# Optimization experiments

Hardware: AMD Instinct MI355X
Metric: run time of the kernel (lower is better)

Reference implementation:

```python
import jax, jax.numpy as jnp
import numpy as np

DIM = 768
N_HEADS = 12
HEAD_DIM = DIM // N_HEADS
SCALE = HEAD_DIM ** -0.5


def setup_inputs() -> dict:
    key = jax.random.key(0)
    ks = jax.random.split(key, 5)
    B, N = 8, 1024
    x = jax.random.normal(ks[0], (B, N, DIM), dtype=jnp.float32)
    # Linear weights stored as (in, out) for x @ W; torch stores (out, in).
    w_qkv = jax.random.normal(ks[1], (DIM, 3 * DIM), dtype=jnp.float32) * (DIM ** -0.5)
    b_qkv = jnp.zeros((3 * DIM,), dtype=jnp.float32)
    w_proj = jax.random.normal(ks[2], (DIM, DIM), dtype=jnp.float32) * (DIM ** -0.5)
    b_proj = jnp.zeros((DIM,), dtype=jnp.float32)
    return {"x": x, "w_qkv": w_qkv, "b_qkv": b_qkv, "w_proj": w_proj, "b_proj": b_proj}


def reference(x, w_qkv, b_qkv, w_proj, b_proj):
    B, N, _ = x.shape
    qkv = x @ w_qkv + b_qkv                       # [B, N, 3*dim]
    qkv = qkv.reshape(B, N, 3, N_HEADS, HEAD_DIM)
    qkv = jnp.transpose(qkv, (2, 0, 3, 1, 4))     # [3, B, H, N, hd]
    q, k, v = qkv[0], qkv[1], qkv[2]
    attn = jnp.einsum("bhqd,bhkd->bhqk", q, k) * SCALE
    attn = jax.nn.softmax(attn, axis=-1)
    out = jnp.einsum("bhqk,bhkd->bhqd", attn, v)  # [B, H, N, hd]
    out = jnp.transpose(out, (0, 2, 1, 3)).reshape(B, N, DIM)
    return out @ w_proj + b_proj
```

## Files before the change

kernel.cpp:

```cpp
#include <hip/hip_runtime.h>
#include <cstdint>

#define DIM 768
#define NH 12
#define HD 64
#define SEQ 1024
#define NBH 96

#define QOFF  ((size_t)0)
#define KOFF  ((size_t)6291456)
#define VOFF  ((size_t)12582912)
#define AOFF  ((size_t)18874368)
#define XOFF  ((size_t)25165824)
#define WQOFF ((size_t)31457280)
#define WPOFF ((size_t)33226752)

#define QSCALE 0.18033688f

#define WAIT_VM8   __builtin_amdgcn_s_waitcnt(0x0F78)
#define WAIT_VM0   __builtin_amdgcn_s_waitcnt(0x0F70)
#define WAIT_LGKM0 __builtin_amdgcn_s_waitcnt(0xC07F)
#define BAR        __builtin_amdgcn_s_barrier()
#define CFENCE     __asm__ __volatile__("" ::: "memory")

typedef __attribute__((ext_vector_type(8))) __bf16 bf16x8;
typedef __attribute__((ext_vector_type(4))) float f32x4;
typedef unsigned short u16;

__device__ __forceinline__ u16 f2bf(float f) {
    union { float f; unsigned u; } x; x.f = f;
    unsigned r = x.u + 0x7fffu + ((x.u >> 16) & 1u);
    return (u16)(r >> 16);
}

__device__ __forceinline__ void async_cp16(const void* g, void* l) {
    __builtin_amdgcn_global_load_lds((const __attribute__((address_space(1))) void*)g,
                                     (__attribute__((address_space(3))) void*)l, 16, 0, 0);
}

__global__ __launch_bounds__(256) void prep(const float* __restrict__ x,
                                            const float* __restrict__ wq,
                                            const float* __restrict__ wp,
                                            u16* __restrict__ ws) {
    const int bid = blockIdx.x;
    const int tid = threadIdx.x;
    if (bid < 6144) {
        int i = bid * 256 + tid;
        float4 v = *(const float4*)&x[(size_t)i * 4];
        ushort4 o; o.x = f2bf(v.x); o.y = f2bf(v.y); o.z = f2bf(v.z); o.w = f2bf(v.w);
        *(ushort4*)&ws[XOFF + (size_t)i * 4] = o;
        return;
    }
    __shared__ float T[64][65];
    const float* w; u16* wt; int N, bx, by;
    if (bid < 6576) { int b = bid - 6144; w = wq; wt = ws + WQOFF; N = 2304; bx = b % 36; by = b / 36; }
    else            { int b = bid - 6576; w = wp; wt = ws + WPOFF; N = 768;  bx = b % 12; by = b / 12; }
    const int K = 768;
    const int k0 = by * 64, n0 = bx * 64;
    const int r = tid >> 4, c4 = (tid & 15) * 4;
#pragma unroll
    for (int i = 0; i < 4; ++i) {
        float4 v = *(const float4*)&w[(size_t)(k0 + r + 16 * i) * N + n0 + c4];
        T[r + 16 * i][c4 + 0] = v.x; T[r + 16 * i][c4 + 1] = v.y;
        T[r + 16 * i][c4 + 2] = v.z; T[r + 16 * i][c4 + 3] = v.w;
    }
    __syncthreads();
#pragma unroll
    for (int i = 0; i < 4; ++i) {
        int rr = r + 16 * i;
        ushort4 o;
        o.x = f2bf(T[c4 + 0][rr]); o.y = f2bf(T[c4 + 1][rr]);
        o.z = f2bf(T[c4 + 2][rr]); o.w = f2bf(T[c4 + 3][rr]);
        *(ushort4*)&wt[(size_t)(n0 + rr) * K + k0 + c4] = o;
    }
}

template <int EPI>
__global__ __launch_bounds__(256) void gemm_bt(const u16* __restrict__ A,
                                               const u16* __restrict__ Bt,
                                               const float* __restrict__ bias,
                                               float* __restrict__ outf,
                                               u16* __restrict__ outq) {
    __shared__ __align__(16) u16 As[2][128 * 64];
    __shared__ __align__(16) u16 Bs[2][128 * 64];
    const int tid = threadIdx.x;
    const int lane = tid & 63;
    const int w = tid >> 6;
    const int wm = w >> 1, wn = w & 1;
    const int m0 = blockIdx.y * 128, n0 = blockIdx.x * 128;

    const int lgrp = lane >> 3;
    const int gg = (lane & 7) ^ lgrp;
    const u16* ga = A  + (size_t)(m0 + w * 32 + lgrp) * 768 + gg * 8;
    const u16* gb = Bt + (size_t)(n0 + w * 32 + lgrp) * 768 + gg * 8;

    const int l15 = lane & 15, qg = lane >> 4, q4 = qg * 4;

    int aoff[4][2], boff[4][2];
#pragma unroll
    for (int r = 0; r < 4; ++r) {
        int row = 64 * wm + 16 * r + l15;
#pragma unroll
        for (int kc = 0; kc < 2; ++kc)
            aoff[r][kc] = row * 64 + (((4 * kc + qg) ^ (row & 7)) << 3);
    }
#pragma unroll
    for (int c = 0; c < 4; ++c) {
        int row = 64 * wn + 16 * c + l15;
#pragma unroll
        for (int kc = 0; kc < 2; ++kc)
            boff[c][kc] = row * 64 + (((4 * kc + qg) ^ (row & 7)) << 3);
    }

#define ISSUE(buf, kk)                                                          \
    {                                                                           \
        _Pragma("unroll")                                                       \
        for (int i = 0; i < 4; ++i) {                                           \
            async_cp16(ga + (size_t)i * 8 * 768 + (kk), &As[buf][w * 2048 + i * 512]); \
            async_cp16(gb + (size_t)i * 8 * 768 + (kk), &Bs[buf][w * 2048 + i * 512]); \
        }                                                                       \
    }

    ISSUE(0, 0)
    ISSUE(1, 64)

    f32x4 acc[4][4] = {};

#pragma unroll
    for (int k = 0; k < 12; ++k) {
        const int cur = k & 1;
        if (k < 11) { WAIT_VM8; } else { WAIT_VM0; }
        BAR;
        CFENCE;
        bf16x8 af[4][2], bfr[4][2];
#pragma unroll
        for (int r = 0; r < 4; ++r)
#pragma unroll
            for (int kc = 0; kc < 2; ++kc) af[r][kc] = *(const bf16x8*)&As[cur][aoff[r][kc]];
#pragma unroll
        for (int c = 0; c < 4; ++c)
#pragma unroll
            for (int kc = 0; kc < 2; ++kc) bfr[c][kc] = *(const bf16x8*)&Bs[cur][boff[c][kc]];
        WAIT_LGKM0;
        CFENCE;
        BAR;
        if (k + 2 < 12) ISSUE(cur, (k + 2) * 64)
#pragma unroll
        for (int kc = 0; kc < 2; ++kc)
#pragma unroll
            for (int r = 0; r < 4; ++r)
#pragma unroll
                for (int c = 0; c < 4; ++c)
                    acc[r][c] = __builtin_amdgcn_mfma_f32_16x16x32_bf16(af[r][kc], bfr[c][kc], acc[r][c], 0, 0, 0);
    }
#undef ISSUE

#pragma unroll
    for (int r = 0; r < 4; ++r) {
#pragma unroll
        for (int c = 0; c < 4; ++c) {
            const int cg = n0 + 64 * wn + 16 * c + l15;
            const float bv = bias[cg];
            const int mb = m0 + 64 * wm + 16 * r + q4;
            if constexpr (EPI == 0) {
#pragma unroll
                for (int g = 0; g < 4; ++g)
                    outf[(size_t)(mb + g) * DIM + cg] = acc[r][c][g] + bv;
            } else {
                const int which = (cg >= 1536) ? 2 : (cg >= 768 ? 1 : 0);
                const int rem = cg - which * 768;
                const int h = rem >> 6, d = rem & 63;
                const int b = mb >> 10, q = mb & 1023;
                if (which == 0) {
#pragma unroll
                    for (int g = 0; g < 4; ++g)
                        outq[QOFF + ((size_t)(b * NH + h) * SEQ + q + g) * HD + d] =
                            f2bf((acc[r][c][g] + bv) * QSCALE);
                } else if (which == 1) {
#pragma unroll
                    for (int g = 0; g < 4; ++g)
                        outq[KOFF + ((size_t)(b * NH + h) * SEQ + q + g) * HD + d] =
                            f2bf(acc[r][c][g] + bv);
                } else {
                    ushort4 pk;
                    pk.x = f2bf(acc[r][c][0] + bv); pk.y = f2bf(acc[r][c][1] + bv);
                    pk.z = f2bf(acc[r][c][2] + bv); pk.w = f2bf(acc[r][c][3] + bv);
                    *(ushort4*)&outq[VOFF + ((size_t)(b * NH + h) * HD + d) * SEQ + q] = pk;
                }
            }
        }
    }
}

__global__ __launch_bounds__(256) void flash_attn(const u16* __restrict__ ws, u16* __restrict__ attn_out) {
    __shared__ __align__(16) u16 Ks[64 * 72];
    __shared__ __align__(16) u16 Vs[64 * 72];
    __shared__ __align__(16) u16 Ps[128 * 72];

    const int tid = threadIdx.x;
    const int lane = tid & 63;
    const int wv = tid >> 6;
    const int qt = blockIdx.x;
    const int bh = blockIdx.y;
    const u16* qp = ws + QOFF + (size_t)bh * SEQ * HD;
    const u16* kp = ws + KOFF + (size_t)bh * SEQ * HD;
    const u16* vp = ws + VOFF + (size_t)bh * HD * SEQ;

    const int l15 = lane & 15, qg = lane >> 4, q8 = qg * 8, q4 = qg * 4;

    bf16x8 bq[2][2];
#pragma unroll
    for (int r = 0; r < 2; ++r)
#pragma unroll
        for (int kc = 0; kc < 2; ++kc)
            bq[r][kc] = *(const bf16x8*)&qp[(size_t)(qt * 128 + 32 * wv + 16 * r + l15) * HD + 32 * kc + q8];

    f32x4 oacc[2][4] = {};
    float lsum[2] = {0.f, 0.f};

    for (int kt = 0; kt < 16; ++kt) {
        __syncthreads();
#pragma unroll
        for (int i = 0; i < 2; ++i) {
            int off = (tid + 256 * i) * 8;
            int row = off >> 6, col = off & 63;
            *(uint4*)&Ks[row * 72 + col] = *(const uint4*)&kp[(size_t)(kt * 64 + row) * HD + col];
            *(uint4*)&Vs[row * 72 + col] = *(const uint4*)&vp[(size_t)row * SEQ + kt * 64 + col];
        }
        __syncthreads();

        f32x4 st[4][2] = {};
#pragma unroll
        for (int c = 0; c < 4; ++c) {
#pragma unroll
            for (int kc = 0; kc < 2; ++kc) {
                bf16x8 ak = *(const bf16x8*)&Ks[(16 * c + l15) * 72 + 32 * kc + q8];
#pragma unroll
                for (int r = 0; r < 2; ++r)
                    st[c][r] = __builtin_amdgcn_mfma_f32_16x16x32_bf16(ak, bq[r][kc], st[c][r], 0, 0, 0);
            }
        }

#pragma unroll
        for (int r = 0; r < 2; ++r) {
#pragma unroll
            for (int c = 0; c < 4; ++c) {
                float p0 = __builtin_amdgcn_exp2f(st[c][r][0]);
                float p1 = __builtin_amdgcn_exp2f(st[c][r][1]);
                float p2 = __builtin_amdgcn_exp2f(st[c][r][2]);
                float p3 = __builtin_amdgcn_exp2f(st[c][r][3]);
                lsum[r] += (p0 + p1) + (p2 + p3);
                ushort4 pk; pk.x = f2bf(p0); pk.y = f2bf(p1); pk.z = f2bf(p2); pk.w = f2bf(p3);
                *(ushort4*)&Ps[(32 * wv + 16 * r + l15) * 72 + 16 * c + q4] = pk;
            }
        }

#pragma unroll
        for (int r = 0; r < 2; ++r) {
#pragma unroll
            for (int kc = 0; kc < 2; ++kc) {
                bf16x8 ap = *(const bf16x8*)&Ps[(32 * wv + 16 * r + l15) * 72 + 32 * kc + q8];
#pragma unroll
                for (int cd = 0; cd < 4; ++cd) {
                    bf16x8 bv = *(const bf16x8*)&Vs[(16 * cd + l15) * 72 + 32 * kc + q8];
                    oacc[r][cd] = __builtin_amdgcn_mfma_f32_16x16x32_bf16(ap, bv, oacc[r][cd], 0, 0, 0);
                }
            }
        }
    }

#pragma unroll
    for (int r = 0; r < 2; ++r) {
        lsum[r] += __shfl_xor(lsum[r], 16);
        lsum[r] += __shfl_xor(lsum[r], 32);
    }
    float linv[2][4];
#pragma unroll
    for (int r = 0; r < 2; ++r)
#pragma unroll
        for (int g = 0; g < 4; ++g)
            linv[r][g] = 1.f / __shfl(lsum[r], q4 + g);

    const int b = bh / NH, h = bh % NH;
#pragma unroll
    for (int r = 0; r < 2; ++r) {
#pragma unroll
        for (int g = 0; g < 4; ++g) {
            int qrow = qt * 128 + 32 * wv + 16 * r + q4 + g;
            size_t grow = (size_t)(b * SEQ + qrow) * DIM + h * HD;
#pragma unroll
            for (int cd = 0; cd < 4; ++cd)
                attn_out[grow + 16 * cd + l15] = f2bf(oacc[r][cd][g] * linv[r][g]);
        }
    }
}

extern "C" void kernel_launch(void* const* d_in, const int* in_sizes, int n_in,
                              void* d_out, int out_size, void* d_ws, size_t ws_size,
                              hipStream_t stream) {
    const float* x      = (const float*)d_in[0];
    const float* w_qkv  = (const float*)d_in[1];
    const float* b_qkv  = (const float*)d_in[2];
    const float* w_proj = (const float*)d_in[3];
    const float* b_proj = (const float*)d_in[4];
    float* out = (float*)d_out;
    u16* ws = (u16*)d_ws;

    prep<<<6720, 256, 0, stream>>>(x, w_qkv, w_proj, ws);
    gemm_bt<1><<<dim3(18, 64), 256, 0, stream>>>(ws + XOFF, ws + WQOFF, b_qkv, nullptr, ws);
    flash_attn<<<dim3(8, 96), 256, 0, stream>>>(ws, ws + AOFF);
    gemm_bt<0><<<dim3(6, 64), 256, 0, stream>>>(ws + AOFF, ws + WPOFF, b_proj, out, nullptr);
}
```

Before: 216.7 us.

## Double-buffer K via async LDS loads, read V directly into registers, swizzle LDS

Flash attention now prefetches the next K tile into a second LDS buffer with global_load_lds while computing the current tile. V fragments are loaded straight from global memory into registers instead of being staged through shared memory. K and P tiles use an XOR-swizzled 64-wide layout instead of padded rows to avoid bank conflicts, and P is packed with a hardware bf16 convert. The aim is to overlap global loads with MFMA work and cut LDS traffic, at the cost of more registers and direct uncached-pattern V reads.

```diff
diff --git a/kernel.cpp b/kernel.cpp
--- a/kernel.cpp
+++ b/kernel.cpp
@@ -24,6 +24,7 @@
 #define CFENCE     __asm__ __volatile__("" ::: "memory")
 
 typedef __attribute__((ext_vector_type(8))) __bf16 bf16x8;
+typedef __attribute__((ext_vector_type(2))) __bf16 bf16x2;
 typedef __attribute__((ext_vector_type(4))) float f32x4;
 typedef unsigned short u16;
 
@@ -31,6 +32,15 @@
     union { float f; unsigned u; } x; x.f = f;
     unsigned r = x.u + 0x7fffu + ((x.u >> 16) & 1u);
     return (u16)(r >> 16);
+}
+
+__device__ __forceinline__ unsigned pkbf(float a, float b) {
+#if __has_builtin(__builtin_amdgcn_cvt_pk_bf16_f32)
+    bf16x2 v = __builtin_amdgcn_cvt_pk_bf16_f32(a, b);
+    union { bf16x2 v; unsigned u; } c; c.v = v; return c.u;
+#else
+    return (unsigned)f2bf(a) | ((unsigned)f2bf(b) << 16);
+#endif
 }
 
 __device__ __forceinline__ void async_cp16(const void* g, void* l) {
@@ -193,9 +203,8 @@
 }
 
 __global__ __launch_bounds__(256) void flash_attn(const u16* __restrict__ ws, u16* __restrict__ attn_out) {
-    __shared__ __align__(16) u16 Ks[64 * 72];
-    __shared__ __align__(16) u16 Vs[64 * 72];
-    __shared__ __align__(16) u16 Ps[128 * 72];
+    __shared__ __align__(16) u16 Ks[2][64 * 64];
+    __shared__ __align__(16) u16 Ps[128 * 64];
 
     const int tid = threadIdx.x;
     const int lane = tid & 63;
@@ -207,6 +216,7 @@
     const u16* vp = ws + VOFF + (size_t)bh * HD * SEQ;
 
     const int l15 = lane & 15, qg = lane >> 4, q8 = qg * 8, q4 = qg * 4;
+    const int l7 = l15 & 7;
 
     bf16x8 bq[2][2];
 #pragma unroll
@@ -214,30 +224,58 @@
 #pragma unroll
         for (int kc = 0; kc < 2; ++kc)
             bq[r][kc] = *(const bf16x8*)&qp[(size_t)(qt * 128 + 32 * wv + 16 * r + l15) * HD + 32 * kc + q8];
+
+    const int lgrp = lane >> 3;
+    const int gg = (lane & 7) ^ lgrp;
+    auto kissue = [&](int buf, int ktv) {
+#pragma unroll
+        for (int i = 0; i < 2; ++i)
+            async_cp16(kp + (size_t)(ktv * 64 + wv * 16 + i * 8 + lgrp) * 64 + gg * 8,
+                       &Ks[buf][(wv * 16 + i * 8) * 64]);
+    };
+    kissue(0, 0);
+
+    int akoff[4][2], apoff[2][2], pwoff[2][4];
+#pragma unroll
+    for (int c = 0; c < 4; ++c)
+#pragma unroll
+        for (int kc = 0; kc < 2; ++kc)
+            akoff[c][kc] = (16 * c + l15) * 64 + (((4 * kc + qg) ^ l7) << 3);
+#pragma unroll
+    for (int r = 0; r < 2; ++r) {
+#pragma unroll
+        for (int kc = 0; kc < 2; ++kc)
+            apoff[r][kc] = (32 * wv + 16 * r + l15) * 64 + (((4 * kc + qg) ^ l7) << 3);
+#pragma unroll
+        for (int c = 0; c < 4; ++c)
+            pwoff[r][c] = (32 * wv + 16 * r + l15) * 64 + (((2 * c + (qg >> 1)) ^ l7) << 3) + (qg & 1) * 4;
+    }
 
     f32x4 oacc[2][4] = {};
     float lsum[2] = {0.f, 0.f};
 
     for (int kt = 0; kt < 16; ++kt) {
-        __syncthreads();
-#pragma unroll
-        for (int i = 0; i < 2; ++i) {
-            int off = (tid + 256 * i) * 8;
-            int row = off >> 6, col = off & 63;
-            *(uint4*)&Ks[row * 72 + col] = *(const uint4*)&kp[(size_t)(kt * 64 + row) * HD + col];
-            *(uint4*)&Vs[row * 72 + col] = *(const uint4*)&vp[(size_t)row * SEQ + kt * 64 + col];
-        }
-        __syncthreads();
-
-        f32x4 st[4][2] = {};
+        const int cur = kt & 1;
+        WAIT_VM0;
+        BAR;
+        CFENCE;
+
+        bf16x8 bv[4][2];
+#pragma unroll
+        for (int cd = 0; cd < 4; ++cd)
+#pragma unroll
+            for (int kc = 0; kc < 2; ++kc)
+                bv[cd][kc] = *(const bf16x8*)&vp[(size_t)(16 * cd + l15) * SEQ + kt * 64 + 32 * kc + q8];
+
+        f32x4 sacc[4][2] = {};
 #pragma unroll
         for (int c = 0; c < 4; ++c) {
 #pragma unroll
             for (int kc = 0; kc < 2; ++kc) {
-                bf16x8 ak = *(const bf16x8*)&Ks[(16 * c + l15) * 72 + 32 * kc + q8];
+                bf16x8 ak = *(const bf16x8*)&Ks[cur][akoff[c][kc]];
 #pragma unroll
                 for (int r = 0; r < 2; ++r)
-                    st[c][r] = __builtin_amdgcn_mfma_f32_16x16x32_bf16(ak, bq[r][kc], st[c][r], 0, 0, 0);
+                    sacc[c][r] = __builtin_amdgcn_mfma_f32_16x16x32_bf16(ak, bq[r][kc], sacc[c][r], 0, 0, 0);
             }
         }
 
@@ -245,26 +283,30 @@
         for (int r = 0; r < 2; ++r) {
 #pragma unroll
             for (int c = 0; c < 4; ++c) {
-                float p0 = __builtin_amdgcn_exp2f(st[c][r][0]);
-                float p1 = __builtin_amdgcn_exp2f(st[c][r][1]);
-                float p2 = __builtin_amdgcn_exp2f(st[c][r][2]);
-                float p3 = __builtin_amdgcn_exp2f(st[c][r][3]);
+                float p0 = __builtin_amdgcn_exp2f(sacc[c][r][0]);
+                float p1 = __builtin_amdgcn_exp2f(sacc[c][r][1]);
+                float p2 = __builtin_amdgcn_exp2f(sacc[c][r][2]);
+                float p3 = __builtin_amdgcn_exp2f(sacc[c][r][3]);
                 lsum[r] += (p0 + p1) + (p2 + p3);
-                ushort4 pk; pk.x = f2bf(p0); pk.y = f2bf(p1); pk.z = f2bf(p2); pk.w = f2bf(p3);
-                *(ushort4*)&Ps[(32 * wv + 16 * r + l15) * 72 + 16 * c + q4] = pk;
+                uint2 pk2; pk2.x = pkbf(p0, p1); pk2.y = pkbf(p2, p3);
+                *(uint2*)&Ps[pwoff[r][c]] = pk2;
             }
         }
 
+        CFENCE;
+        WAIT_LGKM0;
+        BAR;
+        CFENCE;
+        if (kt < 15) kissue(cur ^ 1, kt + 1);
+
 #pragma unroll
         for (int r = 0; r < 2; ++r) {
 #pragma unroll
             for (int kc = 0; kc < 2; ++kc) {
-                bf16x8 ap = *(const bf16x8*)&Ps[(32 * wv + 16 * r + l15) * 72 + 32 * kc + q8];
-#pragma unroll
-                for (int cd = 0; cd < 4; ++cd) {
-                    bf16x8 bv = *(const bf16x8*)&Vs[(16 * cd + l15) * 72 + 32 * kc + q8];
-                    oacc[r][cd] = __builtin_amdgcn_mfma_f32_16x16x32_bf16(ap, bv, oacc[r][cd], 0, 0, 0);
-                }
+                bf16x8 ap = *(const bf16x8*)&Ps[apoff[r][kc]];
+#pragma unroll
+                for (int cd = 0; cd < 4; ++cd)
+                    oacc[r][cd] = __builtin_amdgcn_mfma_f32_16x16x32_bf16(ap, bv[cd][kc], oacc[r][cd], 0, 0, 0);
             }
         }
     }
```

Result: no change. 218.0 us (+0.6%).
